# Performance work log

Measured on AMD Instinct MI355X. Metric: run time of the kernel, lower is better.

## Reference

```python
import jax, jax.numpy as jnp
import numpy as np

DENSE_SIZE = 2048
BATCH = 64
MAX_SPIKES = 1024


def setup_inputs() -> dict:
    key = jax.random.key(0)
    k_w, k_ids, k_ns = jax.random.split(key, 3)
    # weights ~ N(0, 2) as in tf.random_normal_initializer(0., 2., 42)
    W = jax.random.normal(k_w, (DENSE_SIZE, DENSE_SIZE), dtype=jnp.float32) * 2.0
    spike_ids = jax.random.randint(k_ids, (BATCH, MAX_SPIKES), 0, DENSE_SIZE, dtype=jnp.int32)
    num_spikes = jax.random.randint(k_ns, (BATCH,), 0, MAX_SPIKES, dtype=jnp.int32)
    return {"spike_ids": spike_ids, "num_spikes": num_spikes, "W": W}


def reference(spike_ids, num_spikes, W):
    # Dense-weight x binary-sparse-vector matmul:
    # out[b, j] = sum_{i < num_spikes[b]} W[j, spike_ids[b, i]]
    # i.e. gather active columns of W and sum them.
    mask = (jnp.arange(MAX_SPIKES)[None, :] < num_spikes[:, None]).astype(W.dtype)  # [B, S]
    cols = jnp.take(W.T, spike_ids, axis=0)  # [B, S, D] gathered columns (rows of W.T)
    out = jnp.einsum('bs,bsd->bd', mask, cols)  # [B, D]
    return out
```

## Files before the change

kernel.cpp:

```cpp
#include <hip/hip_runtime.h>

#define DENSE 2048
#define BATCH 64
#define MAXS  1024

typedef __attribute__((ext_vector_type(8))) __bf16 bf16x8;
typedef __attribute__((ext_vector_type(4))) float f32x4;


__global__ __launch_bounds__(256) void hist_kernel(const int* __restrict__ ids,
                                                   const int* __restrict__ ns,
                                                   __bf16* __restrict__ Cbf,
                                                   float* __restrict__ out) {
    __shared__ int cnt[DENSE];
    const int b = blockIdx.x;
    const int tid = threadIdx.x;
    #pragma unroll
    for (int k = tid; k < DENSE; k += 256) cnt[k] = 0;
    __syncthreads();
    const int n = ns[b];
    for (int i = tid; i < n; i += 256) {
        atomicAdd(&cnt[ids[b * MAXS + i]], 1);
    }
    __syncthreads();
    const int mt = b >> 4;
    const int bl = b & 15;
    #pragma unroll
    for (int k = tid; k < DENSE; k += 256) {
        const int lane = bl | (((k >> 3) & 3) << 4);
        const size_t off = (size_t)(((k >> 5) * 4 + mt) * 64 + lane) * 8 + (k & 7);
        Cbf[off] = (__bf16)(float)cnt[k];
        out[(size_t)b * DENSE + k] = 0.0f;
    }
}

__global__ __launch_bounds__(256, 3) void spmm_kernel(const float* __restrict__ W,
                                                      const __bf16* __restrict__ Cbf,
                                                      float* __restrict__ out) {
    const int tid  = threadIdx.x;
    const int lane = tid & 63;
    const int wv   = tid >> 6;
    const int j0   = blockIdx.x * 16;
    const int ks4  = blockIdx.y;

    const int ln = lane & 15;
    const int lq = lane >> 4;

    const int step0 = ks4 * 16 + wv * 4;
    const float* wrow = W + (size_t)(j0 + ln) * DENSE;

    f32x4 w0[4], w1[4];
    #pragma unroll
    for (int s = 0; s < 4; ++s) {
        const int kbase = (step0 + s) * 32 + lq * 8;
        w0[s] = __builtin_nontemporal_load((const f32x4*)(wrow + kbase));
        w1[s] = __builtin_nontemporal_load((const f32x4*)(wrow + kbase + 4));
    }
    bf16x8 afr[4][4];
    #pragma unroll
    for (int s = 0; s < 4; ++s) {
        #pragma unroll
        for (int mt = 0; mt < 4; ++mt) {
            afr[s][mt] = *(const bf16x8*)(Cbf + ((size_t)((step0 + s) * 4 + mt) * 64 + lane) * 8);
        }
    }

    bf16x8 wb[4];
    #pragma unroll
    for (int s = 0; s < 4; ++s) {
        #pragma unroll
        for (int i = 0; i < 4; ++i) {
            wb[s][i]     = (__bf16)w0[s][i];
            wb[s][i + 4] = (__bf16)w1[s][i];
        }
    }

    f32x4 acc[4];
    #pragma unroll
    for (int mt = 0; mt < 4; ++mt) acc[mt] = (f32x4)0.0f;
    #pragma unroll
    for (int s = 0; s < 4; ++s) {
        #pragma unroll
        for (int mt = 0; mt < 4; ++mt) {
            acc[mt] = __builtin_amdgcn_mfma_f32_16x16x32_bf16(afr[s][mt], wb[s], acc[mt], 0, 0, 0);
        }
    }

    __shared__ float P[4][4][4][64];
    #pragma unroll
    for (int mt = 0; mt < 4; ++mt) {
        #pragma unroll
        for (int r = 0; r < 4; ++r) {
            P[wv][mt][r][lane] = acc[mt][r];
        }
    }
    __syncthreads();

    const int jloc  = tid & 15;
    const int bpart = tid >> 4;
    const int lsrc  = ((bpart >> 2) << 4) | jloc;
    const int r     = bpart & 3;
    #pragma unroll
    for (int mt = 0; mt < 4; ++mt) {
        const float v = P[0][mt][r][lsrc] + P[1][mt][r][lsrc]
                      + P[2][mt][r][lsrc] + P[3][mt][r][lsrc];
        atomicAdd(&out[(size_t)(mt * 16 + bpart) * DENSE + j0 + jloc], v);
    }
}

extern "C" void kernel_launch(void* const* d_in, const int* in_sizes, int n_in,
                              void* d_out, int out_size, void* d_ws, size_t ws_size,
                              hipStream_t stream) {
    const int*   ids = (const int*)d_in[0];
    const int*   ns  = (const int*)d_in[1];
    const float* W   = (const float*)d_in[2];
    float*  out = (float*)d_out;
    __bf16* Cbf = (__bf16*)d_ws;

    hipLaunchKernelGGL(hist_kernel, dim3(BATCH), dim3(256), 0, stream, ids, ns, Cbf, out);
    hipLaunchKernelGGL(spmm_kernel, dim3(128, 4), dim3(256), 0, stream, W, Cbf, out);
}
```

Baseline: 74.15 us.

## Split K into eight partial buffers and reduce with a separate kernel instead of atomics

Doubles the K-split of the spmm kernel (grid 128x8, two k-steps per wave) and writes per-split partial sums to a workspace buffer instead of atomically adding into the output. A new reduce kernel sums the eight partials into the output, so the histogram kernel no longer zeroes it. The W loads drop their nontemporal hint and the occupancy hint rises to 5. The aim is more blocks in flight and no float atomics, at the cost of an extra launch and about 4 MB of partial-buffer traffic.

New measurement: 75.32 us. No clear change (+1.6%).

```diff
diff --git a/kernel.cpp b/kernel.cpp
--- a/kernel.cpp
+++ b/kernel.cpp
@@ -3,6 +3,8 @@
 #define DENSE 2048
 #define BATCH 64
 #define MAXS  1024
+#define NSPLIT 8
+#define PART_OFF (1 << 20)
 
 typedef __attribute__((ext_vector_type(8))) __bf16 bf16x8;
 typedef __attribute__((ext_vector_type(4))) float f32x4;
@@ -10,8 +12,7 @@
 
 __global__ __launch_bounds__(256) void hist_kernel(const int* __restrict__ ids,
                                                    const int* __restrict__ ns,
-                                                   __bf16* __restrict__ Cbf,
-                                                   float* __restrict__ out) {
+                                                   __bf16* __restrict__ Cbf) {
     __shared__ int cnt[DENSE];
     const int b = blockIdx.x;
     const int tid = threadIdx.x;
@@ -30,13 +31,12 @@
         const int lane = bl | (((k >> 3) & 3) << 4);
         const size_t off = (size_t)(((k >> 5) * 4 + mt) * 64 + lane) * 8 + (k & 7);
         Cbf[off] = (__bf16)(float)cnt[k];
-        out[(size_t)b * DENSE + k] = 0.0f;
     }
 }
 
-__global__ __launch_bounds__(256, 3) void spmm_kernel(const float* __restrict__ W,
+__global__ __launch_bounds__(256, 5) void spmm_kernel(const float* __restrict__ W,
                                                       const __bf16* __restrict__ Cbf,
-                                                      float* __restrict__ out) {
+                                                      float* __restrict__ pws) {
     const int tid  = threadIdx.x;
     const int lane = tid & 63;
     const int wv   = tid >> 6;
@@ -46,28 +46,28 @@
     const int ln = lane & 15;
     const int lq = lane >> 4;
 
-    const int step0 = ks4 * 16 + wv * 4;
+    const int step0 = ks4 * 8 + wv * 2;
     const float* wrow = W + (size_t)(j0 + ln) * DENSE;
 
-    f32x4 w0[4], w1[4];
+    f32x4 w0[2], w1[2];
     #pragma unroll
-    for (int s = 0; s < 4; ++s) {
+    for (int s = 0; s < 2; ++s) {
         const int kbase = (step0 + s) * 32 + lq * 8;
-        w0[s] = __builtin_nontemporal_load((const f32x4*)(wrow + kbase));
-        w1[s] = __builtin_nontemporal_load((const f32x4*)(wrow + kbase + 4));
+        w0[s] = *(const f32x4*)(wrow + kbase);
+        w1[s] = *(const f32x4*)(wrow + kbase + 4);
     }
-    bf16x8 afr[4][4];
+    bf16x8 afr[2][4];
     #pragma unroll
-    for (int s = 0; s < 4; ++s) {
+    for (int s = 0; s < 2; ++s) {
         #pragma unroll
         for (int mt = 0; mt < 4; ++mt) {
             afr[s][mt] = *(const bf16x8*)(Cbf + ((size_t)((step0 + s) * 4 + mt) * 64 + lane) * 8);
         }
     }
 
-    bf16x8 wb[4];
+    bf16x8 wb[2];
     #pragma unroll
-    for (int s = 0; s < 4; ++s) {
+    for (int s = 0; s < 2; ++s) {
         #pragma unroll
         for (int i = 0; i < 4; ++i) {
             wb[s][i]     = (__bf16)w0[s][i];
@@ -79,7 +79,7 @@
     #pragma unroll
     for (int mt = 0; mt < 4; ++mt) acc[mt] = (f32x4)0.0f;
     #pragma unroll
-    for (int s = 0; s < 4; ++s) {
+    for (int s = 0; s < 2; ++s) {
         #pragma unroll
         for (int mt = 0; mt < 4; ++mt) {
             acc[mt] = __builtin_amdgcn_mfma_f32_16x16x32_bf16(afr[s][mt], wb[s], acc[mt], 0, 0, 0);
@@ -100,12 +100,26 @@
     const int bpart = tid >> 4;
     const int lsrc  = ((bpart >> 2) << 4) | jloc;
     const int r     = bpart & 3;
+    float* pd = pws + (size_t)ks4 * (BATCH * DENSE);
     #pragma unroll
     for (int mt = 0; mt < 4; ++mt) {
         const float v = P[0][mt][r][lsrc] + P[1][mt][r][lsrc]
                       + P[2][mt][r][lsrc] + P[3][mt][r][lsrc];
-        atomicAdd(&out[(size_t)(mt * 16 + bpart) * DENSE + j0 + jloc], v);
+        pd[(size_t)(mt * 16 + bpart) * DENSE + j0 + jloc] = v;
     }
+}
+
+__global__ __launch_bounds__(256) void reduce_kernel(const float* __restrict__ pws,
+                                                     float* __restrict__ out) {
+    const int t = blockIdx.x * 256 + threadIdx.x;
+    const size_t i = (size_t)t * 4;
+    f32x4 a = *(const f32x4*)(pws + i);
+    #pragma unroll
+    for (int s = 1; s < NSPLIT; ++s) {
+        const f32x4 v = *(const f32x4*)(pws + (size_t)s * (BATCH * DENSE) + i);
+        a.x += v.x; a.y += v.y; a.z += v.z; a.w += v.w;
+    }
+    *(f32x4*)(out + i) = a;
 }
 
 extern "C" void kernel_launch(void* const* d_in, const int* in_sizes, int n_in,
@@ -116,7 +130,9 @@
     const float* W   = (const float*)d_in[2];
     float*  out = (float*)d_out;
     __bf16* Cbf = (__bf16*)d_ws;
+    float*  pws = (float*)((char*)d_ws + PART_OFF);
 
-    hipLaunchKernelGGL(hist_kernel, dim3(BATCH), dim3(256), 0, stream, ids, ns, Cbf, out);
-    hipLaunchKernelGGL(spmm_kernel, dim3(128, 4), dim3(256), 0, stream, W, Cbf, out);
+    hipLaunchKernelGGL(hist_kernel, dim3(BATCH), dim3(256), 0, stream, ids, ns, Cbf);
+    hipLaunchKernelGGL(spmm_kernel, dim3(128, NSPLIT), dim3(256), 0, stream, W, Cbf, pws);
+    hipLaunchKernelGGL(reduce_kernel, dim3((BATCH * DENSE / 4) / 256), dim3(256), 0, stream, pws, out);
 }
```

## Fuse histogram and SpMM into one cooperative kernel with grid sync and L2 prefetch

Applied to the files above, without the earlier changes.

Replaces the two launches with one cooperative kernel of 256 blocks. The first 64 blocks build the per-batch spike-count histograms while the other blocks zero the output and touch W with strided loads to warm the cache. A grid-wide sync follows, then each block computes a 16-row by half-K slice with a software-pipelined MFMA loop over 8 K steps. The aim is to remove the second launch and overlap the W fetch with the histogram phase, at the cost of a grid barrier and fewer, longer blocks.

New measurement: 121.3 us. +63.6%, slower.

```diff
diff --git a/kernel.cpp b/kernel.cpp
--- a/kernel.cpp
+++ b/kernel.cpp
@@ -1,4 +1,7 @@
 #include <hip/hip_runtime.h>
+#include <hip/hip_cooperative_groups.h>
+
+namespace cg = cooperative_groups;
 
 #define DENSE 2048
 #define BATCH 64
@@ -8,85 +11,100 @@
 typedef __attribute__((ext_vector_type(4))) float f32x4;
 
 
-__global__ __launch_bounds__(256) void hist_kernel(const int* __restrict__ ids,
-                                                   const int* __restrict__ ns,
-                                                   __bf16* __restrict__ Cbf,
-                                                   float* __restrict__ out) {
+__global__ __launch_bounds__(256) void fused_kernel(const int* __restrict__ ids,
+                                                    const int* __restrict__ ns,
+                                                    const float* __restrict__ W,
+                                                    __bf16* __restrict__ Cbf,
+                                                    float* __restrict__ out) {
     __shared__ int cnt[DENSE];
-    const int b = blockIdx.x;
+    __shared__ float P[4][4][4][64];
+
     const int tid = threadIdx.x;
-    #pragma unroll
-    for (int k = tid; k < DENSE; k += 256) cnt[k] = 0;
-    __syncthreads();
-    const int n = ns[b];
-    for (int i = tid; i < n; i += 256) {
-        atomicAdd(&cnt[ids[b * MAXS + i]], 1);
+    const int bid = blockIdx.x;
+
+    if (bid < BATCH) {
+        const int b = bid;
+        #pragma unroll
+        for (int k = tid; k < DENSE; k += 256) cnt[k] = 0;
+        __syncthreads();
+        const int n = ns[b];
+        for (int i = tid; i < n; i += 256) {
+            atomicAdd(&cnt[ids[b * MAXS + i]], 1);
+        }
+        __syncthreads();
+        const int mt = b >> 4;
+        const int bl = b & 15;
+        #pragma unroll
+        for (int k = tid; k < DENSE; k += 256) {
+            const int lane = bl | (((k >> 3) & 3) << 4);
+            const size_t off = (size_t)(((k >> 5) * 4 + mt) * 64 + lane) * 8 + (k & 7);
+            Cbf[off] = (__bf16)(float)cnt[k];
+        }
+    } else {
+        const int t = (bid - BATCH) * 256 + tid;
+        if (t < (BATCH * DENSE) / 4) ((f32x4*)out)[t] = (f32x4)0.0f;
+        float s = 0.0f;
+        for (int i = t; i < (DENSE * DENSE) / 16; i += 192 * 256) {
+            s += W[(size_t)i * 16];
+        }
+        if (s != s) out[0] = s;
     }
-    __syncthreads();
-    const int mt = b >> 4;
-    const int bl = b & 15;
-    #pragma unroll
-    for (int k = tid; k < DENSE; k += 256) {
-        const int lane = bl | (((k >> 3) & 3) << 4);
-        const size_t off = (size_t)(((k >> 5) * 4 + mt) * 64 + lane) * 8 + (k & 7);
-        Cbf[off] = (__bf16)(float)cnt[k];
-        out[(size_t)b * DENSE + k] = 0.0f;
-    }
-}
 
-__global__ __launch_bounds__(256, 3) void spmm_kernel(const float* __restrict__ W,
-                                                      const __bf16* __restrict__ Cbf,
-                                                      float* __restrict__ out) {
-    const int tid  = threadIdx.x;
+    cg::this_grid().sync();
+
     const int lane = tid & 63;
     const int wv   = tid >> 6;
-    const int j0   = blockIdx.x * 16;
-    const int ks4  = blockIdx.y;
+    const int jt   = bid >> 1;
+    const int kh   = bid & 1;
+    const int j0   = jt * 16;
+    const int ln   = lane & 15;
+    const int lq   = lane >> 4;
 
-    const int ln = lane & 15;
-    const int lq = lane >> 4;
-
-    const int step0 = ks4 * 16 + wv * 4;
     const float* wrow = W + (size_t)(j0 + ln) * DENSE;
-
-    f32x4 w0[4], w1[4];
-    #pragma unroll
-    for (int s = 0; s < 4; ++s) {
-        const int kbase = (step0 + s) * 32 + lq * 8;
-        w0[s] = __builtin_nontemporal_load((const f32x4*)(wrow + kbase));
-        w1[s] = __builtin_nontemporal_load((const f32x4*)(wrow + kbase + 4));
-    }
-    bf16x8 afr[4][4];
-    #pragma unroll
-    for (int s = 0; s < 4; ++s) {
-        #pragma unroll
-        for (int mt = 0; mt < 4; ++mt) {
-            afr[s][mt] = *(const bf16x8*)(Cbf + ((size_t)((step0 + s) * 4 + mt) * 64 + lane) * 8);
-        }
-    }
-
-    bf16x8 wb[4];
-    #pragma unroll
-    for (int s = 0; s < 4; ++s) {
-        #pragma unroll
-        for (int i = 0; i < 4; ++i) {
-            wb[s][i]     = (__bf16)w0[s][i];
-            wb[s][i + 4] = (__bf16)w1[s][i];
-        }
-    }
+    const int ks0 = kh * 32 + wv * 8;
 
     f32x4 acc[4];
     #pragma unroll
     for (int mt = 0; mt < 4; ++mt) acc[mt] = (f32x4)0.0f;
+
+    f32x4 cw0, cw1, nw0, nw1;
+    bf16x8 ca[4], na[4];
+
+    {
+        const int kb = ks0 * 32 + lq * 8;
+        cw0 = *(const f32x4*)(wrow + kb);
+        cw1 = *(const f32x4*)(wrow + kb + 4);
+        #pragma unroll
+        for (int mt = 0; mt < 4; ++mt)
+            ca[mt] = *(const bf16x8*)(Cbf + ((size_t)(ks0 * 4 + mt) * 64 + lane) * 8);
+    }
+
     #pragma unroll
-    for (int s = 0; s < 4; ++s) {
+    for (int s = 0; s < 8; ++s) {
+        if (s < 7) {
+            const int ks = ks0 + s + 1;
+            const int kb = ks * 32 + lq * 8;
+            nw0 = *(const f32x4*)(wrow + kb);
+            nw1 = *(const f32x4*)(wrow + kb + 4);
+            #pragma unroll
+            for (int mt = 0; mt < 4; ++mt)
+                na[mt] = *(const bf16x8*)(Cbf + ((size_t)(ks * 4 + mt) * 64 + lane) * 8);
+        }
+        bf16x8 wb;
+        #pragma unroll
+        for (int i = 0; i < 4; ++i) {
+            wb[i]     = (__bf16)cw0[i];
+            wb[i + 4] = (__bf16)cw1[i];
+        }
         #pragma unroll
         for (int mt = 0; mt < 4; ++mt) {
-            acc[mt] = __builtin_amdgcn_mfma_f32_16x16x32_bf16(afr[s][mt], wb[s], acc[mt], 0, 0, 0);
+            acc[mt] = __builtin_amdgcn_mfma_f32_16x16x32_bf16(ca[mt], wb, acc[mt], 0, 0, 0);
         }
+        cw0 = nw0; cw1 = nw1;
+        #pragma unroll
+        for (int mt = 0; mt < 4; ++mt) ca[mt] = na[mt];
     }
 
-    __shared__ float P[4][4][4][64];
     #pragma unroll
     for (int mt = 0; mt < 4; ++mt) {
         #pragma unroll
@@ -117,6 +135,7 @@
     float*  out = (float*)d_out;
     __bf16* Cbf = (__bf16*)d_ws;
 
-    hipLaunchKernelGGL(hist_kernel, dim3(BATCH), dim3(256), 0, stream, ids, ns, Cbf, out);
-    hipLaunchKernelGGL(spmm_kernel, dim3(128, 4), dim3(256), 0, stream, W, Cbf, out);
+    void* args[] = {(void*)&ids, (void*)&ns, (void*)&W, (void*)&Cbf, (void*)&out};
+    hipLaunchCooperativeKernel((const void*)fused_kernel, dim3(256), dim3(256),
+                               args, 0, stream);
 }
```
